# Kernel tuning notes

Measured on AMD Instinct MI355X. Metric: run time of the kernel, lower is better.

Reference implementation:

```python
import jax, jax.numpy as jnp
import numpy as np

N, E = 100000, 1600000
FEAT, HID, MSG, OUT, GOAL = 32, 64, 32, 8, 16
EPS = 1e-5


def _bn(x, gamma, beta):
    # BatchNorm1d in training mode: batch mean + biased variance
    mu = jnp.mean(x, axis=0)
    var = jnp.var(x, axis=0)
    return gamma * (x - mu) * jax.lax.rsqrt(var + EPS) + beta


def setup_inputs() -> dict:
    key = jax.random.key(0)
    ks = jax.random.split(key, 12)
    inp = {
        "nodes": jax.random.normal(ks[0], (N, FEAT), dtype=jnp.float32),
        "goal": jax.random.normal(ks[1], (N, GOAL), dtype=jnp.float32),
        "edge_src": jax.random.randint(ks[2], (E,), 0, N, dtype=jnp.int32),
        "edge_dst": jax.random.randint(ks[3], (E,), 0, N, dtype=jnp.int32),
        "send_input": 1,
        "get_output": 1,
        # InputModel: Linear(FEAT->HID) + ReLU + BN
        "W_in": jax.random.normal(ks[4], (FEAT, HID), dtype=jnp.float32) * 0.1,
        "b_in": jnp.zeros((HID,), dtype=jnp.float32),
        "g_in": jnp.ones((HID,), dtype=jnp.float32),
        "be_in": jnp.zeros((HID,), dtype=jnp.float32),
        # MessageModel: Linear(HID->MSG) + ReLU + BN
        "W_msg": jax.random.normal(ks[5], (HID, MSG), dtype=jnp.float32) * 0.1,
        "b_msg": jnp.zeros((MSG,), dtype=jnp.float32),
        "g_msg": jnp.ones((MSG,), dtype=jnp.float32),
        "be_msg": jnp.zeros((MSG,), dtype=jnp.float32),
        # UpdateModel (goal_opt=1): Linear(MSG+HID+GOAL->HID) + ReLU + BN
        "W_upd": jax.random.normal(ks[6], (MSG + HID + GOAL, HID), dtype=jnp.float32) * 0.1,
        "b_upd": jnp.zeros((HID,), dtype=jnp.float32),
        "g_upd": jnp.ones((HID,), dtype=jnp.float32),
        "be_upd": jnp.zeros((HID,), dtype=jnp.float32),
        # OutputModel (no goal): Linear(HID->OUT)
        "W_out": jax.random.normal(ks[7], (HID, OUT), dtype=jnp.float32) * 0.1,
        "b_out": jnp.zeros((OUT,), dtype=jnp.float32),
    }
    return inp


def reference(nodes, goal, edge_src, edge_dst, send_input, get_output,
              W_in, b_in, g_in, be_in,
              W_msg, b_msg, g_msg, be_msg,
              W_upd, b_upd, g_upd, be_upd,
              W_out, b_out):
    # InputModel
    if send_input:
        h = _bn(jax.nn.relu(nodes @ W_in + b_in), g_in, be_in)  # [N, HID]
    else:
        h = nodes
    # MessageModel
    m = _bn(jax.nn.relu(h @ W_msg + b_msg), g_msg, be_msg)      # [N, MSG]
    # _aggregate: gather predecessor messages, sum per destination node
    agg = jax.ops.segment_sum(m[edge_src], edge_dst, num_segments=N)  # [N, MSG]
    # UpdateModel (goal_opt=1 -> concat goal)
    cat = jnp.concatenate([agg, h, goal], axis=1)               # [N, MSG+HID+GOAL]
    u = _bn(jax.nn.relu(cat @ W_upd + b_upd), g_upd, be_upd)    # [N, HID]
    if get_output:
        out = u @ W_out + b_out                                  # [N, OUT]
        return (u, out)
    return (u, None)
```

## Files before the change

kernel.cpp:

```cpp
#include <hip/hip_runtime.h>

#define NN 100000
#define EE 1600000
#define FEAT 32
#define HID 64
#define MSG 32
#define GOALD 16
#define OUTD 8
#define UPD_IN 112
#define EPS 1e-5f

__global__ __launch_bounds__(256) void k_in_stats(
    const float* __restrict__ nodes, const float* __restrict__ W_in,
    const float* __restrict__ b_in, float* __restrict__ stats1)
{
    __shared__ float red[256];
    const int tid = threadIdx.x;
    const int j = tid & 63, slot = tid >> 6;
    float w[FEAT];
#pragma unroll
    for (int k = 0; k < FEAT; ++k) w[k] = W_in[k * HID + j];
    const float bj = b_in[j];
    float lsum = 0.f, lsq = 0.f;
    for (int i = blockIdx.x * 4 + slot; i < NN; i += gridDim.x * 4) {
        const float4* row = (const float4*)(nodes + (size_t)i * FEAT);
        float acc = bj;
#pragma unroll
        for (int q = 0; q < FEAT / 4; ++q) {
            float4 r = row[q];
            acc = fmaf(r.x, w[q * 4 + 0], acc);
            acc = fmaf(r.y, w[q * 4 + 1], acc);
            acc = fmaf(r.z, w[q * 4 + 2], acc);
            acc = fmaf(r.w, w[q * 4 + 3], acc);
        }
        float v = fmaxf(acc, 0.f);
        lsum += v; lsq += v * v;
    }
    red[tid] = lsum; __syncthreads();
    if (tid < 64) atomicAdd(&stats1[tid], red[tid] + red[tid + 64] + red[tid + 128] + red[tid + 192]);
    __syncthreads();
    red[tid] = lsq; __syncthreads();
    if (tid < 64) atomicAdd(&stats1[64 + tid], red[tid] + red[tid + 64] + red[tid + 128] + red[tid + 192]);
}

__global__ void k_finalize(const float* __restrict__ stats,
                           const float* __restrict__ gamma,
                           const float* __restrict__ beta,
                           float* __restrict__ scsh, int C)
{
    int j = threadIdx.x;
    if (j < C) {
        float mean = stats[j] * (1.f / NN);
        float var  = stats[C + j] * (1.f / NN) - mean * mean;
        float sc = gamma[j] * rsqrtf(var + EPS);
        scsh[j] = sc;
        scsh[C + j] = beta[j] - mean * sc;
    }
}

__global__ __launch_bounds__(256) void k_h_msg(
    const float* __restrict__ nodes, const float* __restrict__ W_in,
    const float* __restrict__ b_in, const float* __restrict__ sc1,
    const float* __restrict__ W_msg, const float* __restrict__ b_msg,
    float* __restrict__ h_out, float* __restrict__ x2_out,
    float* __restrict__ stats2)
{
    __shared__ float shh[4][HID];
    __shared__ float red[256];
    const int tid = threadIdx.x;
    const int j = tid & 63, slot = tid >> 6;
    const int j2 = j & 31, half = j >> 5;
    float w[FEAT];
#pragma unroll
    for (int k = 0; k < FEAT; ++k) w[k] = W_in[k * HID + j];
    float wm[32];
#pragma unroll
    for (int k = 0; k < 32; ++k) wm[k] = W_msg[(half * 32 + k) * MSG + j2];
    const float bj = b_in[j];
    const float s1 = sc1[j], t1 = sc1[HID + j];
    const float bm = b_msg[j2];
    float lsum = 0.f, lsq = 0.f;
    for (int base = blockIdx.x * 4; base < NN; base += gridDim.x * 4) {
        const int i = base + slot;
        const bool act = i < NN;
        float hv = 0.f;
        if (act) {
            const float4* row = (const float4*)(nodes + (size_t)i * FEAT);
            float acc = bj;
#pragma unroll
            for (int q = 0; q < FEAT / 4; ++q) {
                float4 r = row[q];
                acc = fmaf(r.x, w[q * 4 + 0], acc);
                acc = fmaf(r.y, w[q * 4 + 1], acc);
                acc = fmaf(r.z, w[q * 4 + 2], acc);
                acc = fmaf(r.w, w[q * 4 + 3], acc);
            }
            hv = fmaf(fmaxf(acc, 0.f), s1, t1);
            h_out[(size_t)i * HID + j] = hv;
        }
        shh[slot][j] = hv;
        __syncthreads();
        if (act) {
            const float4* hr = (const float4*)(&shh[slot][half * 32]);
            float acc2 = 0.f;
#pragma unroll
            for (int q = 0; q < 8; ++q) {
                float4 r = hr[q];
                acc2 = fmaf(r.x, wm[q * 4 + 0], acc2);
                acc2 = fmaf(r.y, wm[q * 4 + 1], acc2);
                acc2 = fmaf(r.z, wm[q * 4 + 2], acc2);
                acc2 = fmaf(r.w, wm[q * 4 + 3], acc2);
            }
            acc2 += __shfl_xor(acc2, 32);
            if (half == 0) {
                float v = fmaxf(acc2 + bm, 0.f);
                x2_out[(size_t)i * MSG + j2] = v;
                lsum += v; lsq += v * v;
            }
        }
        __syncthreads();
    }
    red[tid] = (half == 0) ? lsum : 0.f; __syncthreads();
    if (tid < 32) atomicAdd(&stats2[tid], red[tid] + red[tid + 64] + red[tid + 128] + red[tid + 192]);
    __syncthreads();
    red[tid] = (half == 0) ? lsq : 0.f; __syncthreads();
    if (tid < 32) atomicAdd(&stats2[32 + tid], red[tid] + red[tid + 64] + red[tid + 128] + red[tid + 192]);
}

__global__ __launch_bounds__(256) void k_edges(
    const int* __restrict__ esrc, const int* __restrict__ edst,
    const float* __restrict__ x2, const float* __restrict__ sc2,
    float* __restrict__ agg)
{
    const int c = threadIdx.x & 31;
    const float s = sc2[c], t = sc2[MSG + c];
    const int total = EE * 32;
    const int stride = gridDim.x * blockDim.x;
    for (int idx = blockIdx.x * blockDim.x + threadIdx.x; idx < total; idx += stride) {
        const int e = idx >> 5;
        const int si = esrc[e], di = edst[e];
        const float v = x2[(size_t)si * MSG + c];
        atomicAdd(&agg[(size_t)di * MSG + c], fmaf(v, s, t));
    }
}

__global__ __launch_bounds__(256) void k_upd(
    const float* __restrict__ agg, const float* __restrict__ h,
    const float* __restrict__ goal, const float* __restrict__ W_upd,
    const float* __restrict__ b_upd, float* __restrict__ x3_out,
    float* __restrict__ stats3)
{
    __shared__ float cat[4][UPD_IN];
    __shared__ float red[256];
    const int tid = threadIdx.x;
    const int j = tid & 63, slot = tid >> 6;
    float w[UPD_IN];
#pragma unroll
    for (int k = 0; k < UPD_IN; ++k) w[k] = W_upd[k * HID + j];
    const float bj = b_upd[j];
    float lsum = 0.f, lsq = 0.f;
    for (int base = blockIdx.x * 4; base < NN; base += gridDim.x * 4) {
        const int i = base + slot;
        const bool act = i < NN;
        if (act) {
            if (j < 32) cat[slot][j] = agg[(size_t)i * MSG + j];
            cat[slot][32 + j] = h[(size_t)i * HID + j];
            if (j < 16) cat[slot][96 + j] = goal[(size_t)i * GOALD + j];
        }
        __syncthreads();
        if (act) {
            const float4* cr = (const float4*)cat[slot];
            float acc = bj;
#pragma unroll
            for (int q = 0; q < UPD_IN / 4; ++q) {
                float4 r = cr[q];
                acc = fmaf(r.x, w[q * 4 + 0], acc);
                acc = fmaf(r.y, w[q * 4 + 1], acc);
                acc = fmaf(r.z, w[q * 4 + 2], acc);
                acc = fmaf(r.w, w[q * 4 + 3], acc);
            }
            float v = fmaxf(acc, 0.f);
            x3_out[(size_t)i * HID + j] = v;
            lsum += v; lsq += v * v;
        }
        __syncthreads();
    }
    red[tid] = lsum; __syncthreads();
    if (tid < 64) atomicAdd(&stats3[tid], red[tid] + red[tid + 64] + red[tid + 128] + red[tid + 192]);
    __syncthreads();
    red[tid] = lsq; __syncthreads();
    if (tid < 64) atomicAdd(&stats3[64 + tid], red[tid] + red[tid + 64] + red[tid + 128] + red[tid + 192]);
}

__global__ __launch_bounds__(256) void k_out(
    float* __restrict__ x3u, const float* __restrict__ sc3,
    const float* __restrict__ W_out, const float* __restrict__ b_out,
    float* __restrict__ o_out)
{
    __shared__ float shu[4][HID];
    const int tid = threadIdx.x;
    const int j = tid & 63, slot = tid >> 6;
    const int o = j & 7, part = j >> 3;
    const float s3 = sc3[j], t3 = sc3[HID + j];
    float w[8];
#pragma unroll
    for (int k = 0; k < 8; ++k) w[k] = W_out[(part * 8 + k) * OUTD + o];
    const float bo = b_out[o];
    for (int base = blockIdx.x * 4; base < NN; base += gridDim.x * 4) {
        const int i = base + slot;
        const bool act = i < NN;
        float u = 0.f;
        if (act) {
            u = fmaf(x3u[(size_t)i * HID + j], s3, t3);
            x3u[(size_t)i * HID + j] = u;
        }
        shu[slot][j] = u;
        __syncthreads();
        if (act) {
            const float* ur = &shu[slot][part * 8];
            float acc = 0.f;
#pragma unroll
            for (int k = 0; k < 8; ++k) acc = fmaf(ur[k], w[k], acc);
            acc += __shfl_xor(acc, 8);
            acc += __shfl_xor(acc, 16);
            acc += __shfl_xor(acc, 32);
            if (part == 0) o_out[(size_t)i * OUTD + o] = acc + bo;
        }
        __syncthreads();
    }
}

extern "C" void kernel_launch(void* const* d_in, const int* in_sizes, int n_in,
                              void* d_out, int out_size, void* d_ws, size_t ws_size,
                              hipStream_t stream)
{
    (void)in_sizes; (void)n_in; (void)out_size;
    const float* nodes  = (const float*)d_in[0];
    const float* goal   = (const float*)d_in[1];
    const int*   esrc   = (const int*)d_in[2];
    const int*   edst   = (const int*)d_in[3];
    const float* W_in   = (const float*)d_in[6];
    const float* b_in   = (const float*)d_in[7];
    const float* g_in   = (const float*)d_in[8];
    const float* be_in  = (const float*)d_in[9];
    const float* W_msg  = (const float*)d_in[10];
    const float* b_msg  = (const float*)d_in[11];
    const float* g_msg  = (const float*)d_in[12];
    const float* be_msg = (const float*)d_in[13];
    const float* W_upd  = (const float*)d_in[14];
    const float* b_upd  = (const float*)d_in[15];
    const float* g_upd  = (const float*)d_in[16];
    const float* be_upd = (const float*)d_in[17];
    const float* W_out  = (const float*)d_in[18];
    const float* b_out  = (const float*)d_in[19];

    const size_t need = ((size_t)NN * 128 + 640) * sizeof(float);
    if (ws_size < need) return;

    float* st = (float*)d_ws;
    float* stats1 = st;
    float* stats2 = st + 128;
    float* stats3 = st + 192;
    float* sc1    = st + 320;
    float* sc2    = st + 448;
    float* sc3    = st + 512;
    float* h   = st + 640;
    float* x2  = h + (size_t)NN * 64;
    float* agg = x2 + (size_t)NN * 32;

    float* u_out = (float*)d_out;
    float* o_out = (float*)d_out + (size_t)NN * HID;

    hipMemsetAsync(st, 0, 320 * sizeof(float), stream);
    hipMemsetAsync(agg, 0, (size_t)NN * MSG * sizeof(float), stream);

    k_in_stats<<<1024, 256, 0, stream>>>(nodes, W_in, b_in, stats1);
    k_finalize<<<1, 64, 0, stream>>>(stats1, g_in, be_in, sc1, HID);
    k_h_msg<<<1024, 256, 0, stream>>>(nodes, W_in, b_in, sc1, W_msg, b_msg, h, x2, stats2);
    k_finalize<<<1, 64, 0, stream>>>(stats2, g_msg, be_msg, sc2, MSG);
    k_edges<<<4096, 256, 0, stream>>>(esrc, edst, x2, sc2, agg);
    k_upd<<<1024, 256, 0, stream>>>(agg, h, goal, W_upd, b_upd, u_out, stats3);
    k_finalize<<<1, 64, 0, stream>>>(stats3, g_upd, be_upd, sc3, HID);
    k_out<<<1024, 256, 0, stream>>>(u_out, sc3, W_out, b_out, o_out);
}
```

Before: 492.1 us.

## Fold BN finalize into consumers and use packed float2 atomics in edge scatter

Removes the three single-block finalize kernels by having each consumer kernel compute its BatchNorm scale and shift directly from the accumulated stats. The edge scatter now handles two channels per thread, with a float2 gather and a packed two-wide global atomic add where the builtin exists. This halves the thread count and atomic instruction count in the heaviest kernel and drops three launches. The cost is redundant per-thread rsqrt work, and a scalar-atomic fallback if the builtin is unavailable.

After: 641.7 us. 30.4% more time.

```diff
diff --git a/kernel.cpp b/kernel.cpp
--- a/kernel.cpp
+++ b/kernel.cpp
@@ -1,4 +1,5 @@
 #include <hip/hip_runtime.h>
+#include <stdint.h>
 
 #define NN 100000
 #define EE 1600000
@@ -10,6 +11,8 @@
 #define UPD_IN 112
 #define EPS 1e-5f
 
+typedef float f32x2 __attribute__((ext_vector_type(2)));
+
 __global__ __launch_bounds__(256) void k_in_stats(
     const float* __restrict__ nodes, const float* __restrict__ W_in,
     const float* __restrict__ b_in, float* __restrict__ stats1)
@@ -43,24 +46,10 @@
     if (tid < 64) atomicAdd(&stats1[64 + tid], red[tid] + red[tid + 64] + red[tid + 128] + red[tid + 192]);
 }
 
-__global__ void k_finalize(const float* __restrict__ stats,
-                           const float* __restrict__ gamma,
-                           const float* __restrict__ beta,
-                           float* __restrict__ scsh, int C)
-{
-    int j = threadIdx.x;
-    if (j < C) {
-        float mean = stats[j] * (1.f / NN);
-        float var  = stats[C + j] * (1.f / NN) - mean * mean;
-        float sc = gamma[j] * rsqrtf(var + EPS);
-        scsh[j] = sc;
-        scsh[C + j] = beta[j] - mean * sc;
-    }
-}
-
 __global__ __launch_bounds__(256) void k_h_msg(
     const float* __restrict__ nodes, const float* __restrict__ W_in,
-    const float* __restrict__ b_in, const float* __restrict__ sc1,
+    const float* __restrict__ b_in, const float* __restrict__ stats1,
+    const float* __restrict__ g_in, const float* __restrict__ be_in,
     const float* __restrict__ W_msg, const float* __restrict__ b_msg,
     float* __restrict__ h_out, float* __restrict__ x2_out,
     float* __restrict__ stats2)
@@ -77,7 +66,10 @@
 #pragma unroll
     for (int k = 0; k < 32; ++k) wm[k] = W_msg[(half * 32 + k) * MSG + j2];
     const float bj = b_in[j];
-    const float s1 = sc1[j], t1 = sc1[HID + j];
+    const float m1 = stats1[j] * (1.f / NN);
+    const float va1 = stats1[HID + j] * (1.f / NN) - m1 * m1;
+    const float s1 = g_in[j] * rsqrtf(va1 + EPS);
+    const float t1 = be_in[j] - m1 * s1;
     const float bm = b_msg[j2];
     float lsum = 0.f, lsq = 0.f;
     for (int base = blockIdx.x * 4; base < NN; base += gridDim.x * 4) {
@@ -129,18 +121,36 @@
 
 __global__ __launch_bounds__(256) void k_edges(
     const int* __restrict__ esrc, const int* __restrict__ edst,
-    const float* __restrict__ x2, const float* __restrict__ sc2,
+    const float* __restrict__ x2, const float* __restrict__ stats2,
+    const float* __restrict__ g_msg, const float* __restrict__ be_msg,
     float* __restrict__ agg)
 {
-    const int c = threadIdx.x & 31;
-    const float s = sc2[c], t = sc2[MSG + c];
-    const int total = EE * 32;
+    const int c0 = (threadIdx.x & 15) << 1;
+    const float m0 = stats2[c0] * (1.f / NN);
+    const float m1 = stats2[c0 + 1] * (1.f / NN);
+    const float va0 = stats2[MSG + c0] * (1.f / NN) - m0 * m0;
+    const float va1 = stats2[MSG + c0 + 1] * (1.f / NN) - m1 * m1;
+    const float s0 = g_msg[c0] * rsqrtf(va0 + EPS);
+    const float s1 = g_msg[c0 + 1] * rsqrtf(va1 + EPS);
+    const float t0 = be_msg[c0] - m0 * s0;
+    const float t1 = be_msg[c0 + 1] - m1 * s1;
+    const int total = EE * 16;
     const int stride = gridDim.x * blockDim.x;
     for (int idx = blockIdx.x * blockDim.x + threadIdx.x; idx < total; idx += stride) {
-        const int e = idx >> 5;
+        const int e = idx >> 4;
         const int si = esrc[e], di = edst[e];
-        const float v = x2[(size_t)si * MSG + c];
-        atomicAdd(&agg[(size_t)di * MSG + c], fmaf(v, s, t));
+        const f32x2 v = *(const f32x2*)(x2 + (size_t)si * MSG + c0);
+        f32x2 d;
+        d.x = fmaf(v.x, s0, t0);
+        d.y = fmaf(v.y, s1, t1);
+        float* p = agg + (size_t)di * MSG + c0;
+#if __has_builtin(__builtin_amdgcn_global_atomic_fadd_v2f32)
+        typedef __attribute__((address_space(1))) f32x2 f32x2_g;
+        __builtin_amdgcn_global_atomic_fadd_v2f32((f32x2_g*)(uintptr_t)p, d);
+#else
+        atomicAdd(p, d.x);
+        atomicAdd(p + 1, d.y);
+#endif
     }
 }
 
@@ -193,7 +203,8 @@
 }
 
 __global__ __launch_bounds__(256) void k_out(
-    float* __restrict__ x3u, const float* __restrict__ sc3,
+    float* __restrict__ x3u, const float* __restrict__ stats3,
+    const float* __restrict__ g_upd, const float* __restrict__ be_upd,
     const float* __restrict__ W_out, const float* __restrict__ b_out,
     float* __restrict__ o_out)
 {
@@ -201,7 +212,10 @@
     const int tid = threadIdx.x;
     const int j = tid & 63, slot = tid >> 6;
     const int o = j & 7, part = j >> 3;
-    const float s3 = sc3[j], t3 = sc3[HID + j];
+    const float m3 = stats3[j] * (1.f / NN);
+    const float va3 = stats3[HID + j] * (1.f / NN) - m3 * m3;
+    const float s3 = g_upd[j] * rsqrtf(va3 + EPS);
+    const float t3 = be_upd[j] - m3 * s3;
     float w[8];
 #pragma unroll
     for (int k = 0; k < 8; ++k) w[k] = W_out[(part * 8 + k) * OUTD + o];
@@ -254,17 +268,14 @@
     const float* W_out  = (const float*)d_in[18];
     const float* b_out  = (const float*)d_in[19];
 
-    const size_t need = ((size_t)NN * 128 + 640) * sizeof(float);
+    const size_t need = ((size_t)NN * 128 + 320) * sizeof(float);
     if (ws_size < need) return;
 
     float* st = (float*)d_ws;
     float* stats1 = st;
     float* stats2 = st + 128;
     float* stats3 = st + 192;
-    float* sc1    = st + 320;
-    float* sc2    = st + 448;
-    float* sc3    = st + 512;
-    float* h   = st + 640;
+    float* h   = st + 320;
     float* x2  = h + (size_t)NN * 64;
     float* agg = x2 + (size_t)NN * 32;
 
@@ -275,11 +286,9 @@
     hipMemsetAsync(agg, 0, (size_t)NN * MSG * sizeof(float), stream);
 
     k_in_stats<<<1024, 256, 0, stream>>>(nodes, W_in, b_in, stats1);
-    k_finalize<<<1, 64, 0, stream>>>(stats1, g_in, be_in, sc1, HID);
-    k_h_msg<<<1024, 256, 0, stream>>>(nodes, W_in, b_in, sc1, W_msg, b_msg, h, x2, stats2);
-    k_finalize<<<1, 64, 0, stream>>>(stats2, g_msg, be_msg, sc2, MSG);
-    k_edges<<<4096, 256, 0, stream>>>(esrc, edst, x2, sc2, agg);
+    k_h_msg<<<1024, 256, 0, stream>>>(nodes, W_in, b_in, stats1, g_in, be_in,
+                                      W_msg, b_msg, h, x2, stats2);
+    k_edges<<<4096, 256, 0, stream>>>(esrc, edst, x2, stats2, g_msg, be_msg, agg);
     k_upd<<<1024, 256, 0, stream>>>(agg, h, goal, W_upd, b_upd, u_out, stats3);
-    k_finalize<<<1, 64, 0, stream>>>(stats3, g_upd, be_upd, sc3, HID);
-    k_out<<<1024, 256, 0, stream>>>(u_out, sc3, W_out, b_out, o_out);
-}
+    k_out<<<1024, 256, 0, stream>>>(u_out, stats3, g_upd, be_upd, W_out, b_out, o_out);
+}
```
